# Optimization experiments

Hardware: AMD Instinct MI355X
Metric: run time of the kernel (lower is better)

The kernel has to match this reference:

```python
import jax, jax.numpy as jnp
import numpy as np

NX, NU, NY, NW = 64, 32, 32, 64
B, T = 256, 2048


def setup_inputs() -> dict:
    key = jax.random.key(0)
    ks = jax.random.split(key, 11)

    def lin_w(k, out_f, in_f):
        # torch.nn.Linear default init scale ~ 1/sqrt(in_f)
        lim = 1.0 / np.sqrt(in_f)
        return jax.random.uniform(k, (out_f, in_f), jnp.float32, -lim, lim)

    return {
        "x_pred": jax.random.normal(ks[0], (B, T, NU), jnp.float32),
        # Y initialized as identity in the module; keep it well-conditioned
        "Y": jnp.eye(NX, dtype=jnp.float32) + 0.01 * jax.random.normal(ks[1], (NX, NX), jnp.float32),
        # lambdas initialized to ones; keep strictly positive
        "lambdas": 1.0 + 0.1 * jax.random.uniform(ks[2], (NW, 1), jnp.float32),
        "A": lin_w(ks[3], NX, NX),
        "B1": lin_w(ks[4], NX, NU),
        "B2": lin_w(ks[5], NX, NW),
        "C1": lin_w(ks[6], NY, NX),
        "D11": lin_w(ks[7], NY, NU),
        "D12": lin_w(ks[8], NY, NW),
        "C2": lin_w(ks[9], NW, NX),
        "D21": lin_w(ks[10], NW, NU),
    }


def reference(x_pred, Y, lambdas, A, B1, B2, C1, D11, D12, C2, D21):
    n_batch, n_sample, _ = x_pred.shape
    nx = A.shape[0]
    Y_inv = jnp.linalg.inv(Y)
    t_inv = 1.0 / jnp.squeeze(lambdas)  # diag of T_inv, [nw]

    x0 = jnp.zeros((n_batch, nx), x_pred.dtype)
    u_seq = jnp.swapaxes(x_pred, 0, 1)  # [T, B, nu]

    def step(x, u):
        # z = (C2_tilde x + D21_tilde u) @ T_inv ; T_inv diagonal -> column scale
        z = (x @ C2.T + u @ D21.T) * t_inv
        w = jnp.tanh(z)
        y_k = x @ C1.T + u @ D11.T + w @ D12.T
        x_next = (x @ A.T + u @ B1.T + w @ B2.T) @ Y_inv
        return x_next, y_k

    x_final, ys = jax.lax.scan(step, x0, u_seq)
    y = jnp.swapaxes(ys, 0, 1)  # [B, T, ny]
    return y, x_final
```

## Files before the change

### kernel.cpp

```cpp
#include <hip/hip_runtime.h>
#include <cstddef>

#define NXS 64
#define NUS 32
#define NYS 32
#define NWS 64
#define BBATCH 256
#define TT  2048

#define WS_YSTG 24576

typedef float v2f __attribute__((ext_vector_type(2)));

__device__ __forceinline__ float fast_tanh(float x) {
    float e = __expf(2.0f * x);
    return 1.0f - 2.0f * __builtin_amdgcn_rcpf(e + 1.0f);
}

template<int CTRL>
__device__ __forceinline__ float dpp_add(float v) {
    int t = __builtin_amdgcn_update_dpp(0, __float_as_int(v), CTRL, 0xF, 0xF, true);
    return v + __int_as_float(t);
}

__device__ __forceinline__ void pk_fma(v2f& acc, v2f x, v2f w) {
    asm("v_pk_fma_f32 %0, %1, %2, %0" : "+v"(acc) : "v"(x), "v"(w));
}

__device__ __forceinline__ void step_barrier() {
    asm volatile("s_waitcnt lgkmcnt(0)\n\ts_barrier" ::: "memory");
}

__global__ __launch_bounds__(1024) void setup_inv_kernel(const float* __restrict__ Y,
                                                         float* __restrict__ ws) {
    __shared__ float M[64 * 129];
    __shared__ float rowk[128];
    __shared__ float ck[64];
    const int tid = threadIdx.x;

    for (int idx = tid; idx < 64 * 64; idx += 1024) {
        int r = idx >> 6, c = idx & 63;
        M[r * 129 + c]      = Y[idx];
        M[r * 129 + 64 + c] = (r == c) ? 1.0f : 0.0f;
    }
    __syncthreads();

    for (int k = 0; k < 64; ++k) {
        float dv = 1.0f / M[k * 129 + k];
        if (tid < 128) rowk[tid] = M[k * 129 + tid] * dv;
        if (tid >= 128 && tid < 192) ck[tid - 128] = M[(tid - 128) * 129 + k];
        __syncthreads();
        for (int idx = tid; idx < 64 * 128; idx += 1024) {
            int r = idx >> 7, c = idx & 127;
            float cur = M[r * 129 + c];
            M[r * 129 + c] = (r == k) ? rowk[c] : cur - ck[r] * rowk[c];
        }
        __syncthreads();
    }
    for (int idx = tid; idx < 4096; idx += 1024) {
        int r = idx >> 6, c = idx & 63;
        ws[WS_YSTG + idx] = M[r * 129 + 64 + c];
    }
}

__global__ __launch_bounds__(256) void setup_gxw_kernel(const float* __restrict__ lam,
                                                        const float* __restrict__ A,
                                                        const float* __restrict__ B1,
                                                        const float* __restrict__ B2,
                                                        const float* __restrict__ C2,
                                                        const float* __restrict__ D21,
                                                        float* __restrict__ ws) {
    __shared__ float Yi[64 * 64];
    __shared__ float WxT[160 * 64];
    const int tid = threadIdx.x;
    const int bid = blockIdx.x;

    for (int idx = tid; idx < 4096; idx += 256) Yi[idx] = ws[WS_YSTG + idx];
    __syncthreads();

    for (int idx = tid; idx < 10240; idx += 256) {
        int k = idx >> 6, j = idx & 63;
        float s = 0.0f;
        if (k < 64) {
            #pragma unroll 8
            for (int m = 0; m < 64; ++m) s += A[m * 64 + k] * Yi[m * 64 + j];
        } else if (k < 96) {
            int ku = k - 64;
            #pragma unroll 8
            for (int m = 0; m < 64; ++m) s += B1[m * 32 + ku] * Yi[m * 64 + j];
        } else {
            int kw = k - 96;
            #pragma unroll 8
            for (int m = 0; m < 64; ++m) s += B2[m * 64 + kw] * Yi[m * 64 + j];
        }
        WxT[idx] = s;
    }
    __syncthreads();

    for (int idx = bid * 1536 + tid; idx < bid * 1536 + 1536; idx += 256) {
        int c = idx / 192;
        int k = idx - c * 192;
        int km = (k < 64) ? k : (k < 128) ? (96 + k - 64) : (64 + k - 128);
        float v;
        if (c < 64) {
            if (k < 160) {
                float s = 0.0f;
                #pragma unroll 8
                for (int m = 0; m < 64; ++m) s += WxT[km * 64 + m] * C2[c * 64 + m];
                v = s / lam[c];
            } else {
                v = D21[c * 32 + (k - 160)] / lam[c];
            }
        } else {
            int j = c - 64;
            v = (k < 160) ? WxT[km * 64 + j] : 0.0f;
        }
        ws[c * 192 + k] = v;
    }
}

__global__ __launch_bounds__(256) void setup_y_kernel(const float* __restrict__ C1,
                                                      const float* __restrict__ D11,
                                                      const float* __restrict__ D12,
                                                      float* __restrict__ ws) {
    for (int idx = blockIdx.x * 256 + threadIdx.x; idx < 6144; idx += 16 * 256) {
        int c = 128 + idx / 192;
        int k = idx % 192;
        int j = c - 128;
        float v = (k < 64)  ? C1[j * 64 + k]
                : (k < 128) ? D12[j * 64 + (k - 64)]
                : (k < 160) ? D11[j * 32 + (k - 128)]
                            : 0.0f;
        ws[c * 192 + k] = v;
    }
}

__global__ __launch_bounds__(512, 2) void rnn7_kernel(const float* __restrict__ xp,
                                                      const float* __restrict__ ws,
                                                      float* __restrict__ out) {
    const int b   = blockIdx.x;
    const int tid = threadIdx.x;

    __shared__ __align__(16) float sbuf[2][160];
    __shared__ __align__(16) float uRs[32][36];

    const float4* __restrict__ xp4 = (const float4*)(xp + (size_t)b * (TT * NUS));
    const size_t yb   = (size_t)b * (TT * NYS);
    const size_t xoff = (size_t)BBATCH * TT * NYS;

    if (tid < 256) {
        int s = tid >> 3, q8 = tid & 7;
        float4 v = make_float4(0.f, 0.f, 0.f, 0.f);
        if (s < 31) v = xp4[s * 8 + q8];
        *(float4*)&uRs[s][q8 * 4] = v;
    }
    if (tid < 160) sbuf[0][tid] = 0.0f;
    __syncthreads();

    const int e  = tid & 7;
    const int Gq = tid >> 3;

    const int NOUT = (Gq < 32) ? 3 : 2;
    v2f w[3][12];
    #pragma unroll
    for (int r = 0; r < 3; ++r) {
        if (r >= NOUT) break;
        const int col = (r == 0) ? Gq : (r == 1) ? (64 + Gq) : (128 + Gq);
        const float* Gc = ws + (size_t)col * 192;
        const float* sb = Gc + 16 * e;
        #pragma unroll
        for (int k = 0; k < 4; ++k) {
            float4 gv = *(const float4*)(sb + 4 * k);
            w[r][2 * k]     = (v2f){gv.x, gv.y};
            w[r][2 * k + 1] = (v2f){gv.z, gv.w};
        }
        const float* ub = Gc + ((e < 4) ? (128 + 8 * e) : (160 + 8 * (e - 4)));
        #pragma unroll
        for (int t = 0; t < 2; ++t) {
            float4 gv = *(const float4*)(ub + 4 * t);
            w[r][8 + 2 * t] = (v2f){gv.x, gv.y};
            w[r][9 + 2 * t] = (v2f){gv.z, gv.w};
        }
    }

    const int wr_off = (e == 0) ? (((64 + Gq) >> 4) * 20 + ((64 + Gq) & 15))
                                : ((Gq >> 4) * 20 + (Gq & 15));

    float ybat[8];
    float lastx = 0.0f;
    float4 upref = make_float4(0.f, 0.f, 0.f, 0.f);

    auto dostep = [&](int rb, int wb, int ip, int ic,
                      float& s0o, float& s1o, float& s2o) {
        const float4* sv4 = (const float4*)(&sbuf[rb][0] + e * 20);
        float4 s0 = sv4[0], s1 = sv4[1], s2 = sv4[2], s3 = sv4[3];
        const float4* uu = (const float4*)&uRs[(e < 4) ? ip : ic][8 * (e & 3)];
        float4 u0 = uu[0], u1 = uu[1];
        v2f sv[12] = {{s0.x, s0.y}, {s0.z, s0.w}, {s1.x, s1.y}, {s1.z, s1.w},
                      {s2.x, s2.y}, {s2.z, s2.w}, {s3.x, s3.y}, {s3.z, s3.w},
                      {u0.x, u0.y}, {u0.z, u0.w}, {u1.x, u1.y}, {u1.z, u1.w}};
        float sr[3] = {0.f, 0.f, 0.f};
        #pragma unroll
        for (int r = 0; r < 3; ++r) {
            if (r >= NOUT) break;
            v2f acc = (v2f){0.f, 0.f};
            #pragma unroll
            for (int k = 0; k < 12; ++k) pk_fma(acc, sv[k], w[r][k]);
            float s = acc.x + acc.y;
            s = dpp_add<0xB1>(s);
            s = dpp_add<0x4E>(s);
            s = dpp_add<0x141>(s);
            sr[r] = s;
        }
        if (e < 2) {
            float val = (e == 0) ? fast_tanh(sr[0]) : sr[1];
            sbuf[wb][wr_off] = val;
        }
        s0o = sr[0]; s1o = sr[1]; s2o = sr[2];
    };

    {
        float a, bv, c;
        dostep(0, 1, 31, 0, a, bv, c);
    }
    step_barrier();

    #pragma unroll 8
    for (int i = 0; i < TT; ++i) {
        const int rp = (i + 1) & 1, wp = i & 1;
        if ((i & 15) == 0) {
            int t = i + 16 + (tid >> 3);
            if (tid < 128 && t < TT) upref = xp4[t * 8 + (tid & 7)];
        }
        if ((i & 15) == 8) {
            int t = i + 8 + (tid >> 3);
            if (tid < 128 && t < TT) *(float4*)&uRs[t & 31][(tid & 7) * 4] = upref;
        }
        float sr0, sr1, sr2;
        dostep(rp, wp, i & 31, (i + 1) & 31, sr0, sr1, sr2);
        lastx = sr1;
        if (NOUT == 3 && e == 2) {
            ybat[i & 7] = sr2;
            if ((i & 7) == 7) {
                size_t base = yb + (size_t)(i - 7) * NYS + Gq;
                #pragma unroll
                for (int ss = 0; ss < 8; ++ss) out[base + (size_t)ss * NYS] = ybat[ss];
            }
        }
        step_barrier();
    }

    if (e == 1) out[xoff + (size_t)b * 64 + Gq] = lastx;
}

extern "C" void kernel_launch(void* const* d_in, const int* in_sizes, int n_in,
                              void* d_out, int out_size, void* d_ws, size_t ws_size,
                              hipStream_t stream) {
    const float* xp  = (const float*)d_in[0];
    const float* Y   = (const float*)d_in[1];
    const float* lam = (const float*)d_in[2];
    const float* A   = (const float*)d_in[3];
    const float* B1  = (const float*)d_in[4];
    const float* B2  = (const float*)d_in[5];
    const float* C1  = (const float*)d_in[6];
    const float* D11 = (const float*)d_in[7];
    const float* D12 = (const float*)d_in[8];
    const float* C2  = (const float*)d_in[9];
    const float* D21 = (const float*)d_in[10];
    float* out = (float*)d_out;
    float* ws  = (float*)d_ws;

    hipLaunchKernelGGL(setup_inv_kernel, dim3(1),  dim3(1024), 0, stream, Y, ws);
    hipLaunchKernelGGL(setup_gxw_kernel, dim3(16), dim3(256),  0, stream,
                       lam, A, B1, B2, C2, D21, ws);
    hipLaunchKernelGGL(setup_y_kernel,   dim3(16), dim3(256),  0, stream,
                       C1, D11, D12, ws);
    hipLaunchKernelGGL(rnn7_kernel, dim3(BBATCH), dim3(512), 0, stream, xp, ws, out);
}
```

Before: 916.7 us.

## Pack two batch chains per block, prefetch inputs, split FMA accumulators

The recurrent kernel now runs two independent batch sequences in each 1024-thread block, with per-chain shared buffers, and launches half as many blocks. The LDS read of the next step's input is moved before the step barrier so it is off the dependent path. Each dot product uses two packed-FMA accumulator chains instead of one to shorten the serial FMA dependency. The aim is to hide per-step latency by interleaving two chains, at the risk of a wider barrier across 16 waves and only half the CUs being occupied.

```diff
diff --git a/kernel.cpp b/kernel.cpp
--- a/kernel.cpp
+++ b/kernel.cpp
@@ -135,30 +135,32 @@
     }
 }
 
-__global__ __launch_bounds__(512, 2) void rnn7_kernel(const float* __restrict__ xp,
-                                                      const float* __restrict__ ws,
-                                                      float* __restrict__ out) {
-    const int b   = blockIdx.x;
+__global__ __launch_bounds__(1024, 4) void rnn8_kernel(const float* __restrict__ xp,
+                                                       const float* __restrict__ ws,
+                                                       float* __restrict__ out) {
     const int tid = threadIdx.x;
-
-    __shared__ __align__(16) float sbuf[2][160];
-    __shared__ __align__(16) float uRs[32][36];
+    const int ch  = tid >> 9;
+    const int t   = tid & 511;
+    const int b   = blockIdx.x * 2 + ch;
+
+    __shared__ __align__(16) float sbuf[2][2][160];
+    __shared__ __align__(16) float uRs[2][32][36];
 
     const float4* __restrict__ xp4 = (const float4*)(xp + (size_t)b * (TT * NUS));
     const size_t yb   = (size_t)b * (TT * NYS);
     const size_t xoff = (size_t)BBATCH * TT * NYS;
 
-    if (tid < 256) {
-        int s = tid >> 3, q8 = tid & 7;
+    if (t < 256) {
+        int s = t >> 3, q8 = t & 7;
         float4 v = make_float4(0.f, 0.f, 0.f, 0.f);
         if (s < 31) v = xp4[s * 8 + q8];
-        *(float4*)&uRs[s][q8 * 4] = v;
-    }
-    if (tid < 160) sbuf[0][tid] = 0.0f;
-    __syncthreads();
-
-    const int e  = tid & 7;
-    const int Gq = tid >> 3;
+        *(float4*)&uRs[ch][s][q8 * 4] = v;
+    }
+    if (t < 160) sbuf[ch][0][t] = 0.0f;
+    __syncthreads();
+
+    const int e  = t & 7;
+    const int Gq = t >> 3;
 
     const int NOUT = (Gq < 32) ? 3 : 2;
     v2f w[3][12];
@@ -176,10 +178,10 @@
         }
         const float* ub = Gc + ((e < 4) ? (128 + 8 * e) : (160 + 8 * (e - 4)));
         #pragma unroll
-        for (int t = 0; t < 2; ++t) {
-            float4 gv = *(const float4*)(ub + 4 * t);
-            w[r][8 + 2 * t] = (v2f){gv.x, gv.y};
-            w[r][9 + 2 * t] = (v2f){gv.z, gv.w};
+        for (int tt = 0; tt < 2; ++tt) {
+            float4 gv = *(const float4*)(ub + 4 * tt);
+            w[r][8 + 2 * tt] = (v2f){gv.x, gv.y};
+            w[r][9 + 2 * tt] = (v2f){gv.z, gv.w};
         }
     }
 
@@ -189,24 +191,30 @@
     float ybat[8];
     float lastx = 0.0f;
     float4 upref = make_float4(0.f, 0.f, 0.f, 0.f);
-
-    auto dostep = [&](int rb, int wb, int ip, int ic,
-                      float& s0o, float& s1o, float& s2o) {
-        const float4* sv4 = (const float4*)(&sbuf[rb][0] + e * 20);
+    float4 u0r, u1r;
+
+    auto uread = [&](int ip, int ic) {
+        const float4* uu = (const float4*)&uRs[ch][(e < 4) ? ip : ic][8 * (e & 3)];
+        u0r = uu[0]; u1r = uu[1];
+    };
+
+    auto dostep = [&](int rb, int wb, float& s0o, float& s1o, float& s2o) {
+        const float4* sv4 = (const float4*)(&sbuf[ch][rb][0] + e * 20);
         float4 s0 = sv4[0], s1 = sv4[1], s2 = sv4[2], s3 = sv4[3];
-        const float4* uu = (const float4*)&uRs[(e < 4) ? ip : ic][8 * (e & 3)];
-        float4 u0 = uu[0], u1 = uu[1];
         v2f sv[12] = {{s0.x, s0.y}, {s0.z, s0.w}, {s1.x, s1.y}, {s1.z, s1.w},
                       {s2.x, s2.y}, {s2.z, s2.w}, {s3.x, s3.y}, {s3.z, s3.w},
-                      {u0.x, u0.y}, {u0.z, u0.w}, {u1.x, u1.y}, {u1.z, u1.w}};
+                      {u0r.x, u0r.y}, {u0r.z, u0r.w}, {u1r.x, u1r.y}, {u1r.z, u1r.w}};
         float sr[3] = {0.f, 0.f, 0.f};
         #pragma unroll
         for (int r = 0; r < 3; ++r) {
             if (r >= NOUT) break;
-            v2f acc = (v2f){0.f, 0.f};
+            v2f acc = (v2f){0.f, 0.f}, acc2 = (v2f){0.f, 0.f};
             #pragma unroll
-            for (int k = 0; k < 12; ++k) pk_fma(acc, sv[k], w[r][k]);
-            float s = acc.x + acc.y;
+            for (int k = 0; k < 6; ++k)  pk_fma(acc,  sv[k],     w[r][k]);
+            #pragma unroll
+            for (int k = 0; k < 6; ++k)  pk_fma(acc2, sv[6 + k], w[r][6 + k]);
+            v2f a = acc + acc2;
+            float s = a.x + a.y;
             s = dpp_add<0xB1>(s);
             s = dpp_add<0x4E>(s);
             s = dpp_add<0x141>(s);
@@ -214,14 +222,16 @@
         }
         if (e < 2) {
             float val = (e == 0) ? fast_tanh(sr[0]) : sr[1];
-            sbuf[wb][wr_off] = val;
+            sbuf[ch][wb][wr_off] = val;
         }
         s0o = sr[0]; s1o = sr[1]; s2o = sr[2];
     };
 
     {
+        uread(31, 0);
         float a, bv, c;
-        dostep(0, 1, 31, 0, a, bv, c);
+        dostep(0, 1, a, bv, c);
+        uread(0, 1);
     }
     step_barrier();
 
@@ -229,15 +239,15 @@
     for (int i = 0; i < TT; ++i) {
         const int rp = (i + 1) & 1, wp = i & 1;
         if ((i & 15) == 0) {
-            int t = i + 16 + (tid >> 3);
-            if (tid < 128 && t < TT) upref = xp4[t * 8 + (tid & 7)];
+            int tt = i + 16 + (t >> 3);
+            if (t < 128 && tt < TT) upref = xp4[tt * 8 + (t & 7)];
         }
         if ((i & 15) == 8) {
-            int t = i + 8 + (tid >> 3);
-            if (tid < 128 && t < TT) *(float4*)&uRs[t & 31][(tid & 7) * 4] = upref;
+            int tt = i + 8 + (t >> 3);
+            if (t < 128 && tt < TT) *(float4*)&uRs[ch][tt & 31][(t & 7) * 4] = upref;
         }
         float sr0, sr1, sr2;
-        dostep(rp, wp, i & 31, (i + 1) & 31, sr0, sr1, sr2);
+        dostep(rp, wp, sr0, sr1, sr2);
         lastx = sr1;
         if (NOUT == 3 && e == 2) {
             ybat[i & 7] = sr2;
@@ -247,6 +257,7 @@
                 for (int ss = 0; ss < 8; ++ss) out[base + (size_t)ss * NYS] = ybat[ss];
             }
         }
+        uread((i + 1) & 31, (i + 2) & 31);
         step_barrier();
     }
 
@@ -275,5 +286,6 @@
                        lam, A, B1, B2, C2, D21, ws);
     hipLaunchKernelGGL(setup_y_kernel,   dim3(16), dim3(256),  0, stream,
                        C1, D11, D12, ws);
-    hipLaunchKernelGGL(rnn7_kernel, dim3(BBATCH), dim3(512), 0, stream, xp, ws, out);
-}
+    hipLaunchKernelGGL(rnn8_kernel, dim3(BBATCH / 2), dim3(1024), 0, stream,
+                       xp, ws, out);
+}
```

Result: slower. 1.547 ms (+68.7%).
